# Kernel optimization log

Measured on AMD Instinct MI355X. Metric: run time of the kernel, lower is better.

## Reference

```python
import jax, jax.numpy as jnp
import numpy as np

B, F, R, C = 16384, 256, 32, 16
H1, H2 = 128, 32        # FS-MLP hidden sizes
G1, G2 = 256, 64        # consequent MLP hidden sizes


def setup_inputs() -> dict:
    key = jax.random.key(0)
    ks = jax.random.split(key, 16)
    s = 0.05
    return {
        "data": jax.random.normal(ks[0], (B, F), jnp.float32),
        # per-rule antecedent params (torch inits proto=0, var=1; randomize proto for a nontrivial test)
        "proto": jax.random.normal(ks[1], (R, F), jnp.float32) * 0.1,
        "var": jnp.full((R, F), 0.05, jnp.float32),
        # shared FS-MLP: Linear(F,128)->ReLU->Linear(128,32)->ReLU->Linear(32,1)->ReLU
        "Wf1": jax.random.normal(ks[2], (H1, F), jnp.float32) * s,
        "bf1": jax.random.normal(ks[3], (H1,), jnp.float32) * s,
        "Wf2": jax.random.normal(ks[4], (H2, H1), jnp.float32) * s,
        "bf2": jax.random.normal(ks[5], (H2,), jnp.float32) * s,
        "Wf3": jax.random.normal(ks[6], (1, H2), jnp.float32) * s,
        "bf3": jax.random.normal(ks[7], (1,), jnp.float32) * s,
        # per-rule consequent MLP (stacked over rule dim): Linear(F,256)->ELU->Linear(256,64)->ELU->Linear(64,C)
        "Wc1": jax.random.normal(ks[8], (R, G1, F), jnp.float32) * s,
        "bc1": jax.random.normal(ks[9], (R, G1), jnp.float32) * s,
        "Wc2": jax.random.normal(ks[10], (R, G2, G1), jnp.float32) * s,
        "bc2": jax.random.normal(ks[11], (R, G2), jnp.float32) * s,
        "Wc3": jax.random.normal(ks[12], (R, C, G2), jnp.float32) * s,
        "bc3": jax.random.normal(ks[13], (R, C), jnp.float32) * s,
    }


def reference(data, proto, var, Wf1, bf1, Wf2, bf2, Wf3, bf3,
              Wc1, bc1, Wc2, bc2, Wc3, bc3):
    # Antecedent: Gaussian membership per rule -> [R, B, F]
    v = jnp.clip(var, 1e-4, 0.1)
    mem = jnp.exp(-(data[None, :, :] - proto[:, None, :]) ** 2
                  / (2.0 * v[:, None, :] ** 2))
    # Shared firing-strength MLP on each rule's membership tensor -> [R, B]
    h = jax.nn.relu(jnp.einsum('rbf,of->rbo', mem, Wf1) + bf1)
    h = jax.nn.relu(jnp.einsum('rbo,po->rbp', h, Wf2) + bf2)
    fs_ini = jax.nn.relu(jnp.einsum('rbp,qp->rbq', h, Wf3) + bf3)[..., 0]
    fire_strength = jax.nn.softmax(fs_ini.T, axis=1)  # [B, R], softmax over rules
    # Per-rule consequent MLPs on raw data (batched over rule dim) -> [R, B, C]
    c = jax.nn.elu(jnp.einsum('bf,rhf->rbh', data, Wc1) + bc1[:, None, :])
    c = jax.nn.elu(jnp.einsum('rbh,rgh->rbg', c, Wc2) + bc2[:, None, :])
    c = jax.nn.relu(jnp.einsum('rbg,rcg->rbc', c, Wc3) + bc3[:, None, :])
    # Softmax-weighted sum over rules -> [B, C]
    outputs = jnp.einsum('rbc,br->bc', c, fire_strength)
    return outputs, fire_strength
```

## Files before the change

kernel.cpp:

```cpp
#include <hip/hip_runtime.h>
#include <hip/hip_bf16.h>

#define BN 16384
#define FN 256
#define RN 32
#define CN 16
#define H1N 128
#define H2N 32
#define G1N 256
#define G2N 64

typedef __bf16 bf16_t;
typedef __bf16 bf16x8 __attribute__((ext_vector_type(8)));
typedef __bf16 bf16x4 __attribute__((ext_vector_type(4)));
typedef float f32x4 __attribute__((ext_vector_type(4)));

#define OFF_DATA   0UL
#define OFF_WF1    8388608UL
#define OFF_WF2    8454144UL
#define OFF_WC1    8462336UL
#define OFF_WC2    12656640UL
#define OFF_WC3    13705216UL
#define OFF_FSINI  13770752UL
#define OFF_C3     15867904UL

__device__ __forceinline__ f32x4 mfma16(bf16x8 a, bf16x8 b, f32x4 c) {
  return __builtin_amdgcn_mfma_f32_16x16x32_bf16(a, b, c, 0, 0, 0);
}

__device__ __forceinline__ float elu_f(float v) {
  float e = __builtin_amdgcn_exp2f(v * 1.44269504f) - 1.0f;
  return v > 0.f ? v : e;
}

__device__ __forceinline__ bf16x8 lfrag(const char* base, int strideB, int n0, int k0, int lane) {
  int row = n0 + (lane & 15);
  int off = (k0 * 2 + ((lane >> 4) << 4)) ^ ((row & 7) << 4);
  return *(const bf16x8*)(base + row * strideB + off);
}

__device__ __forceinline__ void pack_frag8(const float* __restrict__ src, bf16_t* __restrict__ dst,
                                           int NT, int KS, int g) {
  int per = NT * KS * 64;
  int r = g / per;
  int local = g - r * per;
  int lane = local & 63;
  int fr = local >> 6;
  int ks = fr / NT;
  int nt = fr - ks * NT;
  int N = NT * 16, K = KS * 32;
  int n = nt * 16 + (lane & 15);
  int k = ks * 32 + ((lane >> 4) << 3);
  const float* s = src + (long)r * N * K + (long)n * K + k;
  float4 a = *(const float4*)s;
  float4 b = *(const float4*)(s + 4);
  bf16x8 o;
  o[0] = (bf16_t)a.x; o[1] = (bf16_t)a.y; o[2] = (bf16_t)a.z; o[3] = (bf16_t)a.w;
  o[4] = (bf16_t)b.x; o[5] = (bf16_t)b.y; o[6] = (bf16_t)b.z; o[7] = (bf16_t)b.w;
  *(bf16x8*)(dst + (long)g * 8) = o;
}

#define G_DATA 524288
#define G_WC1  262144
#define G_WC2  65536
#define G_WF1  4096
#define G_WC3  4096
#define G_WF2  512
#define G_TOTAL (G_DATA + G_WC1 + G_WC2 + G_WF1 + G_WC3 + G_WF2)

__global__ __launch_bounds__(256) void k0_pack(
    const float* __restrict__ data, const float* __restrict__ Wf1, const float* __restrict__ Wf2,
    const float* __restrict__ Wc1, const float* __restrict__ Wc2, const float* __restrict__ Wc3,
    char* __restrict__ ws)
{
  int g = blockIdx.x * 256 + threadIdx.x;
  if (g < G_DATA) {
    const float* s = data + (long)g * 8;
    float4 a = *(const float4*)s, b = *(const float4*)(s + 4);
    bf16x8 o;
    o[0] = (bf16_t)a.x; o[1] = (bf16_t)a.y; o[2] = (bf16_t)a.z; o[3] = (bf16_t)a.w;
    o[4] = (bf16_t)b.x; o[5] = (bf16_t)b.y; o[6] = (bf16_t)b.z; o[7] = (bf16_t)b.w;
    *(bf16x8*)((bf16_t*)(ws + OFF_DATA) + (long)g * 8) = o;
    return;
  }
  g -= G_DATA;
  if (g < G_WC1) { pack_frag8(Wc1, (bf16_t*)(ws + OFF_WC1), 16, 8, g); return; }
  g -= G_WC1;
  if (g < G_WC2) { pack_frag8(Wc2, (bf16_t*)(ws + OFF_WC2), 4, 8, g); return; }
  g -= G_WC2;
  if (g < G_WF1) { pack_frag8(Wf1, (bf16_t*)(ws + OFF_WF1), 8, 8, g); return; }
  g -= G_WF1;
  if (g < G_WC3) { pack_frag8(Wc3, (bf16_t*)(ws + OFF_WC3), 1, 2, g); return; }
  g -= G_WC3;
  if (g < G_WF2) { pack_frag8(Wf2, (bf16_t*)(ws + OFF_WF2), 2, 4, g); return; }
}

__global__ __launch_bounds__(512) void k1_fs(
    const float* __restrict__ data, const float* __restrict__ proto, const float* __restrict__ var,
    const float* __restrict__ bf1g, const float* __restrict__ bf2g,
    const float* __restrict__ Wf3g, const float* __restrict__ bf3g,
    const bf16_t* __restrict__ Wf1p, const bf16_t* __restrict__ Wf2p,
    float* __restrict__ fsini)
{
  __shared__ float proto_s[4][FN];
  __shared__ float ivar_s[4][FN];
  __shared__ __attribute__((aligned(16))) char fs_lds[36864];

  const int bid = blockIdx.x;
  const int rg  = bid >> 8;
  const int b0  = (bid & 255) << 6;
  const int tid = threadIdx.x;
  const int lane = tid & 63;
  const int w   = tid >> 6;

  #pragma unroll
  for (int k = 0; k < 2; ++k) {
    int idx = tid + k * 512;
    int rr = idx >> 8, f = idx & 255;
    int r = rg * 4 + rr;
    proto_s[rr][f] = proto[r * FN + f];
    float v = var[r * FN + f];
    v = fminf(fmaxf(v, 1e-4f), 0.1f);
    ivar_s[rr][f] = 1.4426950408889634f * 0.5f / (v * v);
  }

  const int row = tid >> 3;
  const int f0  = (tid & 7) << 5;
  float4 dreg[8];
  {
    const float* dp = data + (long)(b0 + row) * FN + f0;
    #pragma unroll
    for (int i = 0; i < 8; ++i) dreg[i] = *(const float4*)(dp + i * 4);
  }
  __syncthreads();

  bf16_t* h2t = (bf16_t*)(fs_lds + 32768);
  char* mrow = fs_lds + row * 512;
  const int sw = (row & 7) << 4;

  for (int rr = 0; rr < 4; ++rr) {
    const int r = rg * 4 + rr;

    {
      #pragma unroll
      for (int i = 0; i < 4; ++i) {
        const int f = f0 + i * 8;
        float4 x0 = dreg[i * 2];
        float4 x1 = dreg[i * 2 + 1];
        bf16x8 m; float d;
        d = x0.x - proto_s[rr][f + 0]; m[0] = (bf16_t)__builtin_amdgcn_exp2f(-d * d * ivar_s[rr][f + 0]);
        d = x0.y - proto_s[rr][f + 1]; m[1] = (bf16_t)__builtin_amdgcn_exp2f(-d * d * ivar_s[rr][f + 1]);
        d = x0.z - proto_s[rr][f + 2]; m[2] = (bf16_t)__builtin_amdgcn_exp2f(-d * d * ivar_s[rr][f + 2]);
        d = x0.w - proto_s[rr][f + 3]; m[3] = (bf16_t)__builtin_amdgcn_exp2f(-d * d * ivar_s[rr][f + 3]);
        d = x1.x - proto_s[rr][f + 4]; m[4] = (bf16_t)__builtin_amdgcn_exp2f(-d * d * ivar_s[rr][f + 4]);
        d = x1.y - proto_s[rr][f + 5]; m[5] = (bf16_t)__builtin_amdgcn_exp2f(-d * d * ivar_s[rr][f + 5]);
        d = x1.z - proto_s[rr][f + 6]; m[6] = (bf16_t)__builtin_amdgcn_exp2f(-d * d * ivar_s[rr][f + 6]);
        d = x1.w - proto_s[rr][f + 7]; m[7] = (bf16_t)__builtin_amdgcn_exp2f(-d * d * ivar_s[rr][f + 7]);
        *(bf16x8*)(mrow + ((f * 2) ^ sw)) = m;
      }
    }
    __syncthreads();

    const int mg = w >> 1;
    const int ng = w & 1;
    f32x4 acc[2][2] = {};
    #pragma unroll
    for (int ks = 0; ks < 8; ++ks) {
      bf16x8 a[2], bb[2];
      #pragma unroll
      for (int i = 0; i < 2; ++i)
        a[i] = *(const bf16x8*)(Wf1p + (((ks * 8 + mg * 2 + i) * 64 + lane)) * 8);
      #pragma unroll
      for (int j = 0; j < 2; ++j)
        bb[j] = lfrag(fs_lds, 512, (ng * 2 + j) * 16, ks * 32, lane);
      #pragma unroll
      for (int i = 0; i < 2; ++i)
        #pragma unroll
        for (int j = 0; j < 2; ++j)
          acc[i][j] = mfma16(a[i], bb[j], acc[i][j]);
    }
    __syncthreads();

    #pragma unroll
    for (int i = 0; i < 2; ++i) {
      const int hb = (mg * 2 + i) * 16 + ((lane >> 4) << 2);
      f32x4 bias = *(const f32x4*)(bf1g + hb);
      #pragma unroll
      for (int j = 0; j < 2; ++j) {
        const int b = (ng * 2 + j) * 16 + (lane & 15);
        bf16x4 o;
        #pragma unroll
        for (int q = 0; q < 4; ++q)
          o[q] = (bf16_t)fmaxf(acc[i][j][q] + bias[q], 0.f);
        *(bf16x4*)(fs_lds + b * 256 + ((hb * 2) ^ ((b & 7) << 4))) = o;
      }
    }
    __syncthreads();

    {
      const int m = w >> 2;
      const int n = w & 3;
      f32x4 acc2 = {};
      #pragma unroll
      for (int ks = 0; ks < 4; ++ks) {
        bf16x8 a = *(const bf16x8*)(Wf2p + (((ks * 2 + m) * 64 + lane)) * 8);
        bf16x8 bb = lfrag(fs_lds, 256, n * 16, ks * 32, lane);
        acc2 = mfma16(a, bb, acc2);
      }
      const int p0 = m * 16 + ((lane >> 4) << 2);
      const int b  = n * 16 + (lane & 15);
      f32x4 bias = *(const f32x4*)(bf2g + p0);
      #pragma unroll
      for (int q = 0; q < 4; ++q)
        h2t[(p0 + q) * 64 + b] = (bf16_t)fmaxf(acc2[q] + bias[q], 0.f);
    }
    __syncthreads();

    if (tid < 64) {
      float s = bf3g[0];
      #pragma unroll
      for (int p = 0; p < H2N; ++p) s += (float)h2t[p * 64 + tid] * Wf3g[p];
      fsini[(long)(b0 + tid) * RN + r] = fmaxf(s, 0.f);
    }
    __syncthreads();
  }
}

__global__ __launch_bounds__(256) void k2_softmax(const float* __restrict__ fsini,
                                                  float* __restrict__ fire)
{
  int b = blockIdx.x * 256 + threadIdx.x;
  float v[RN];
  const float4* p = (const float4*)(fsini + (long)b * RN);
  #pragma unroll
  for (int i = 0; i < RN / 4; ++i) {
    float4 t = p[i];
    v[4 * i] = t.x; v[4 * i + 1] = t.y; v[4 * i + 2] = t.z; v[4 * i + 3] = t.w;
  }
  float m = v[0];
  #pragma unroll
  for (int i = 1; i < RN; ++i) m = fmaxf(m, v[i]);
  float s = 0.f;
  #pragma unroll
  for (int i = 0; i < RN; ++i) { v[i] = expf(v[i] - m); s += v[i]; }
  float inv = 1.f / s;
  float4* o = (float4*)(fire + (long)b * RN);
  #pragma unroll
  for (int i = 0; i < RN / 4; ++i) {
    float4 t; t.x = v[4 * i] * inv; t.y = v[4 * i + 1] * inv;
    t.z = v[4 * i + 2] * inv; t.w = v[4 * i + 3] * inv;
    o[i] = t;
  }
}

__global__ __launch_bounds__(512) void k3_cons(
    const bf16_t* __restrict__ datab,
    const bf16_t* __restrict__ Wc1p, const bf16_t* __restrict__ Wc2p, const bf16_t* __restrict__ Wc3p,
    const float* __restrict__ bc1, const float* __restrict__ bc2, const float* __restrict__ bc3,
    float* __restrict__ c3buf)
{
  __shared__ __attribute__((aligned(16))) char a_lds[64 * 512];
  __shared__ __attribute__((aligned(16))) char c2_lds[64 * 128];

  const int bid = blockIdx.x;
  const int xcd = bid & 7;
  const int kk  = bid >> 3;
  const int r   = xcd * 4 + (kk >> 8);
  const int b0  = (kk & 255) << 6;

  const int tid = threadIdx.x;
  const int lane = tid & 63;
  const int w   = tid >> 6;

  {
    const int row = tid >> 3;
    const int e0  = (tid & 7) << 5;
    const bf16_t* sp = datab + (long)(b0 + row) * FN + e0;
    char* drow = a_lds + row * 512;
    const int sw = (row & 7) << 4;
    #pragma unroll
    for (int i = 0; i < 4; ++i) {
      bf16x8 v = *(const bf16x8*)(sp + i * 8);
      *(bf16x8*)(drow + (((e0 + i * 8) * 2) ^ sw)) = v;
    }
  }
  __syncthreads();

  const int wm = w >> 1;
  const int wn = w & 1;
  const bf16_t* W1 = Wc1p + (long)r * G1N * FN;
  f32x4 acc[4][2] = {};
  __builtin_amdgcn_s_setprio(1);
  #pragma unroll
  for (int ks = 0; ks < 8; ++ks) {
    bf16x8 a[4], bb[2];
    #pragma unroll
    for (int i = 0; i < 4; ++i)
      a[i] = *(const bf16x8*)(W1 + (((ks * 16 + wm * 4 + i) * 64 + lane)) * 8);
    #pragma unroll
    for (int j = 0; j < 2; ++j)
      bb[j] = lfrag(a_lds, 512, (wn * 2 + j) * 16, ks * 32, lane);
    #pragma unroll
    for (int i = 0; i < 4; ++i)
      #pragma unroll
      for (int j = 0; j < 2; ++j)
        acc[i][j] = mfma16(a[i], bb[j], acc[i][j]);
  }
  __builtin_amdgcn_s_setprio(0);
  __syncthreads();

  #pragma unroll
  for (int i = 0; i < 4; ++i) {
    const int g1b = (wm * 4 + i) * 16 + ((lane >> 4) << 2);
    f32x4 bias = *(const f32x4*)(bc1 + r * G1N + g1b);
    #pragma unroll
    for (int j = 0; j < 2; ++j) {
      const int b = (wn * 2 + j) * 16 + (lane & 15);
      bf16x4 o;
      #pragma unroll
      for (int q = 0; q < 4; ++q)
        o[q] = (bf16_t)elu_f(acc[i][j][q] + bias[q]);
      *(bf16x4*)(a_lds + b * 512 + ((g1b * 2) ^ ((b & 7) << 4))) = o;
    }
  }
  __syncthreads();

  const int m2 = w >> 1;
  const int n2 = w & 1;
  const bf16_t* W2 = Wc2p + (long)r * G2N * G1N;
  f32x4 acc2[2] = {};
  __builtin_amdgcn_s_setprio(1);
  #pragma unroll
  for (int ks = 0; ks < 8; ++ks) {
    bf16x8 a = *(const bf16x8*)(W2 + (((ks * 4 + m2) * 64 + lane)) * 8);
    #pragma unroll
    for (int j = 0; j < 2; ++j) {
      bf16x8 bb = lfrag(a_lds, 512, (n2 * 2 + j) * 16, ks * 32, lane);
      acc2[j] = mfma16(a, bb, acc2[j]);
    }
  }
  __builtin_amdgcn_s_setprio(0);
  {
    const int g2b = m2 * 16 + ((lane >> 4) << 2);
    f32x4 bias = *(const f32x4*)(bc2 + r * G2N + g2b);
    #pragma unroll
    for (int j = 0; j < 2; ++j) {
      const int b = (n2 * 2 + j) * 16 + (lane & 15);
      bf16x4 o;
      #pragma unroll
      for (int q = 0; q < 4; ++q)
        o[q] = (bf16_t)elu_f(acc2[j][q] + bias[q]);
      *(bf16x4*)(c2_lds + b * 128 + ((g2b * 2) ^ ((b & 7) << 4))) = o;
    }
  }
  __syncthreads();

  if (w < 4) {
    const bf16_t* W3 = Wc3p + (long)r * CN * G2N;
    f32x4 acc3 = {};
    #pragma unroll
    for (int ks = 0; ks < 2; ++ks) {
      bf16x8 a = *(const bf16x8*)(W3 + (((long)ks * 64 + lane)) * 8);
      bf16x8 bb = lfrag(c2_lds, 128, w * 16, ks * 32, lane);
      acc3 = mfma16(a, bb, acc3);
    }
    const int c0 = ((lane >> 4) << 2);
    const int b  = w * 16 + (lane & 15);
    f32x4 bias = *(const f32x4*)(bc3 + r * CN + c0);
    f32x4 o;
    #pragma unroll
    for (int q = 0; q < 4; ++q) o[q] = fmaxf(acc3[q] + bias[q], 0.f);
    *(f32x4*)(c3buf + ((long)r * BN + b0 + b) * CN + c0) = o;
  }
}

__global__ __launch_bounds__(256) void k4_out(const float* __restrict__ c3buf,
                                              const float* __restrict__ fire,
                                              float* __restrict__ out)
{
  int t = blockIdx.x * 256 + threadIdx.x;
  int b = t >> 2, c4 = (t & 3) << 2;
  const float* fp = fire + (long)b * RN;
  f32x4 s = {};
  #pragma unroll
  for (int rr = 0; rr < RN; ++rr) {
    float fw = fp[rr];
    f32x4 v = *(const f32x4*)(c3buf + ((long)rr * BN + b) * CN + c4);
    s += fw * v;
  }
  *(f32x4*)(out + (long)b * CN + c4) = s;
}

extern "C" void kernel_launch(void* const* d_in, const int* in_sizes, int n_in,
                              void* d_out, int out_size, void* d_ws, size_t ws_size,
                              hipStream_t stream) {
  const float* data = (const float*)d_in[0];
  const float* proto = (const float*)d_in[1];
  const float* var  = (const float*)d_in[2];
  const float* Wf1  = (const float*)d_in[3];
  const float* bf1  = (const float*)d_in[4];
  const float* Wf2  = (const float*)d_in[5];
  const float* bf2  = (const float*)d_in[6];
  const float* Wf3  = (const float*)d_in[7];
  const float* bf3  = (const float*)d_in[8];
  const float* Wc1  = (const float*)d_in[9];
  const float* bc1  = (const float*)d_in[10];
  const float* Wc2  = (const float*)d_in[11];
  const float* bc2  = (const float*)d_in[12];
  const float* Wc3  = (const float*)d_in[13];
  const float* bc3  = (const float*)d_in[14];

  char* ws = (char*)d_ws;
  bf16_t* datab = (bf16_t*)(ws + OFF_DATA);
  bf16_t* Wf1p  = (bf16_t*)(ws + OFF_WF1);
  bf16_t* Wf2p  = (bf16_t*)(ws + OFF_WF2);
  bf16_t* Wc1p  = (bf16_t*)(ws + OFF_WC1);
  bf16_t* Wc2p  = (bf16_t*)(ws + OFF_WC2);
  bf16_t* Wc3p  = (bf16_t*)(ws + OFF_WC3);
  float*  fsini = (float*)(ws + OFF_FSINI);
  float*  c3buf = (float*)(ws + OFF_C3);

  float* out  = (float*)d_out;
  float* fire = out + (long)BN * CN;

  k0_pack<<<G_TOTAL / 256, 256, 0, stream>>>(data, Wf1, Wf2, Wc1, Wc2, Wc3, ws);
  k1_fs<<<8 * (BN / 64), 512, 0, stream>>>(data, proto, var, bf1, bf2, Wf3, bf3,
                                           Wf1p, Wf2p, fsini);
  k2_softmax<<<BN / 256, 256, 0, stream>>>(fsini, fire);
  k3_cons<<<RN * (BN / 64), 512, 0, stream>>>(datab, Wc1p, Wc2p, Wc3p, bc1, bc2, bc3, c3buf);
  k4_out<<<(BN * CN / 4) / 256, 256, 0, stream>>>(c3buf, fire, out);
}
```

Before: 262.2 us.

## Merge firing-strength and consequent kernels into one launch with shared LDS

Combines the independent antecedent firing-strength kernel and the per-rule consequent MLP kernel into a single launch, with block ID ranges choosing which body runs. Both bodies share one LDS buffer, and the h2t scratch region is moved to overlap the membership area. The aim is to remove a launch and the tail idle time between the two kernels, letting their work overlap on the GPU. It also removes the s_setprio hints in the consequent GEMMs. The k1 LDS layout change (h2t at offset 16384 inside fs_lds) risks clobbering membership data if that region is still live.

```diff
diff --git a/kernel.cpp b/kernel.cpp
--- a/kernel.cpp
+++ b/kernel.cpp
@@ -23,6 +23,9 @@
 #define OFF_WC3    13705216UL
 #define OFF_FSINI  13770752UL
 #define OFF_C3     15867904UL
+
+#define K1_BLOCKS 2048
+#define K3_BLOCKS 8192
 
 __device__ __forceinline__ f32x4 mfma16(bf16x8 a, bf16x8 b, f32x4 c) {
   return __builtin_amdgcn_mfma_f32_16x16x32_bf16(a, b, c, 0, 0, 0);
@@ -95,18 +98,19 @@
   if (g < G_WF2) { pack_frag8(Wf2, (bf16_t*)(ws + OFF_WF2), 2, 4, g); return; }
 }
 
-__global__ __launch_bounds__(512) void k1_fs(
+__device__ __forceinline__ void k1_body(
+    char* smem, int bid,
     const float* __restrict__ data, const float* __restrict__ proto, const float* __restrict__ var,
     const float* __restrict__ bf1g, const float* __restrict__ bf2g,
     const float* __restrict__ Wf3g, const float* __restrict__ bf3g,
     const bf16_t* __restrict__ Wf1p, const bf16_t* __restrict__ Wf2p,
     float* __restrict__ fsini)
 {
-  __shared__ float proto_s[4][FN];
-  __shared__ float ivar_s[4][FN];
-  __shared__ __attribute__((aligned(16))) char fs_lds[36864];
-
-  const int bid = blockIdx.x;
+  char* fs_lds = smem;
+  float (*proto_s)[FN] = (float(*)[FN])(smem + 32768);
+  float (*ivar_s)[FN]  = (float(*)[FN])(smem + 36864);
+  bf16_t* h2t = (bf16_t*)(fs_lds + 16384);
+
   const int rg  = bid >> 8;
   const int b0  = (bid & 255) << 6;
   const int tid = threadIdx.x;
@@ -134,7 +138,6 @@
   }
   __syncthreads();
 
-  bf16_t* h2t = (bf16_t*)(fs_lds + 32768);
   char* mrow = fs_lds + row * 512;
   const int sw = (row & 7) << 4;
 
@@ -226,43 +229,16 @@
   }
 }
 
-__global__ __launch_bounds__(256) void k2_softmax(const float* __restrict__ fsini,
-                                                  float* __restrict__ fire)
-{
-  int b = blockIdx.x * 256 + threadIdx.x;
-  float v[RN];
-  const float4* p = (const float4*)(fsini + (long)b * RN);
-  #pragma unroll
-  for (int i = 0; i < RN / 4; ++i) {
-    float4 t = p[i];
-    v[4 * i] = t.x; v[4 * i + 1] = t.y; v[4 * i + 2] = t.z; v[4 * i + 3] = t.w;
-  }
-  float m = v[0];
-  #pragma unroll
-  for (int i = 1; i < RN; ++i) m = fmaxf(m, v[i]);
-  float s = 0.f;
-  #pragma unroll
-  for (int i = 0; i < RN; ++i) { v[i] = expf(v[i] - m); s += v[i]; }
-  float inv = 1.f / s;
-  float4* o = (float4*)(fire + (long)b * RN);
-  #pragma unroll
-  for (int i = 0; i < RN / 4; ++i) {
-    float4 t; t.x = v[4 * i] * inv; t.y = v[4 * i + 1] * inv;
-    t.z = v[4 * i + 2] * inv; t.w = v[4 * i + 3] * inv;
-    o[i] = t;
-  }
-}
-
-__global__ __launch_bounds__(512) void k3_cons(
+__device__ __forceinline__ void k3_body(
+    char* smem, int bid,
     const bf16_t* __restrict__ datab,
     const bf16_t* __restrict__ Wc1p, const bf16_t* __restrict__ Wc2p, const bf16_t* __restrict__ Wc3p,
     const float* __restrict__ bc1, const float* __restrict__ bc2, const float* __restrict__ bc3,
     float* __restrict__ c3buf)
 {
-  __shared__ __attribute__((aligned(16))) char a_lds[64 * 512];
-  __shared__ __attribute__((aligned(16))) char c2_lds[64 * 128];
-
-  const int bid = blockIdx.x;
+  char* a_lds  = smem;
+  char* c2_lds = smem + 32768;
+
   const int xcd = bid & 7;
   const int kk  = bid >> 3;
   const int r   = xcd * 4 + (kk >> 8);
@@ -290,7 +266,6 @@
   const int wn = w & 1;
   const bf16_t* W1 = Wc1p + (long)r * G1N * FN;
   f32x4 acc[4][2] = {};
-  __builtin_amdgcn_s_setprio(1);
   #pragma unroll
   for (int ks = 0; ks < 8; ++ks) {
     bf16x8 a[4], bb[2];
@@ -306,7 +281,6 @@
       for (int j = 0; j < 2; ++j)
         acc[i][j] = mfma16(a[i], bb[j], acc[i][j]);
   }
-  __builtin_amdgcn_s_setprio(0);
   __syncthreads();
 
   #pragma unroll
@@ -329,7 +303,6 @@
   const int n2 = w & 1;
   const bf16_t* W2 = Wc2p + (long)r * G2N * G1N;
   f32x4 acc2[2] = {};
-  __builtin_amdgcn_s_setprio(1);
   #pragma unroll
   for (int ks = 0; ks < 8; ++ks) {
     bf16x8 a = *(const bf16x8*)(W2 + (((ks * 4 + m2) * 64 + lane)) * 8);
@@ -339,7 +312,6 @@
       acc2[j] = mfma16(a, bb, acc2[j]);
     }
   }
-  __builtin_amdgcn_s_setprio(0);
   {
     const int g2b = m2 * 16 + ((lane >> 4) << 2);
     f32x4 bias = *(const f32x4*)(bc2 + r * G2N + g2b);
@@ -371,6 +343,53 @@
     #pragma unroll
     for (int q = 0; q < 4; ++q) o[q] = fmaxf(acc3[q] + bias[q], 0.f);
     *(f32x4*)(c3buf + ((long)r * BN + b0 + b) * CN + c0) = o;
+  }
+}
+
+__global__ __launch_bounds__(512) void k13_fused(
+    const float* __restrict__ data, const float* __restrict__ proto, const float* __restrict__ var,
+    const float* __restrict__ bf1g, const float* __restrict__ bf2g,
+    const float* __restrict__ Wf3g, const float* __restrict__ bf3g,
+    const bf16_t* __restrict__ Wf1p, const bf16_t* __restrict__ Wf2p,
+    float* __restrict__ fsini,
+    const bf16_t* __restrict__ datab,
+    const bf16_t* __restrict__ Wc1p, const bf16_t* __restrict__ Wc2p, const bf16_t* __restrict__ Wc3p,
+    const float* __restrict__ bc1, const float* __restrict__ bc2, const float* __restrict__ bc3,
+    float* __restrict__ c3buf)
+{
+  __shared__ __attribute__((aligned(16))) char smem[40960];
+  const int bid = blockIdx.x;
+  if (bid < K1_BLOCKS) {
+    k1_body(smem, bid, data, proto, var, bf1g, bf2g, Wf3g, bf3g, Wf1p, Wf2p, fsini);
+  } else {
+    k3_body(smem, bid - K1_BLOCKS, datab, Wc1p, Wc2p, Wc3p, bc1, bc2, bc3, c3buf);
+  }
+}
+
+__global__ __launch_bounds__(256) void k2_softmax(const float* __restrict__ fsini,
+                                                  float* __restrict__ fire)
+{
+  int b = blockIdx.x * 256 + threadIdx.x;
+  float v[RN];
+  const float4* p = (const float4*)(fsini + (long)b * RN);
+  #pragma unroll
+  for (int i = 0; i < RN / 4; ++i) {
+    float4 t = p[i];
+    v[4 * i] = t.x; v[4 * i + 1] = t.y; v[4 * i + 2] = t.z; v[4 * i + 3] = t.w;
+  }
+  float m = v[0];
+  #pragma unroll
+  for (int i = 1; i < RN; ++i) m = fmaxf(m, v[i]);
+  float s = 0.f;
+  #pragma unroll
+  for (int i = 0; i < RN; ++i) { v[i] = expf(v[i] - m); s += v[i]; }
+  float inv = 1.f / s;
+  float4* o = (float4*)(fire + (long)b * RN);
+  #pragma unroll
+  for (int i = 0; i < RN / 4; ++i) {
+    float4 t; t.x = v[4 * i] * inv; t.y = v[4 * i + 1] * inv;
+    t.z = v[4 * i + 2] * inv; t.w = v[4 * i + 3] * inv;
+    o[i] = t;
   }
 }
 
@@ -424,9 +443,9 @@
   float* fire = out + (long)BN * CN;
 
   k0_pack<<<G_TOTAL / 256, 256, 0, stream>>>(data, Wf1, Wf2, Wc1, Wc2, Wc3, ws);
-  k1_fs<<<8 * (BN / 64), 512, 0, stream>>>(data, proto, var, bf1, bf2, Wf3, bf3,
-                                           Wf1p, Wf2p, fsini);
+  k13_fused<<<K1_BLOCKS + K3_BLOCKS, 512, 0, stream>>>(
+      data, proto, var, bf1, bf2, Wf3, bf3, Wf1p, Wf2p, fsini,
+      datab, Wc1p, Wc2p, Wc3p, bc1, bc2, bc3, c3buf);
   k2_softmax<<<BN / 256, 256, 0, stream>>>(fsini, fire);
-  k3_cons<<<RN * (BN / 64), 512, 0, stream>>>(datab, Wc1p, Wc2p, Wc3p, bc1, bc2, bc3, c3buf);
   k4_out<<<(BN * CN / 4) / 256, 256, 0, stream>>>(c3buf, fire, out);
 }
```

Result: slower. 309.6 us (+18.1%).
